# Kernel tuning notes

Hardware: AMD Instinct MI355X
Metric: run time of the kernel (lower is better)

## Reference

```python
import jax, jax.numpy as jnp
import numpy as np

N_NODES = 100000
D_IN = 64
D_OUT = 64
N_EDGES = 1250000


def setup_inputs() -> dict:
    key = jax.random.key(0)
    k_x, k_e, k_wl, k_bl, k_wr = jax.random.split(key, 5)
    x = jax.random.normal(k_x, (N_NODES, D_IN), dtype=jnp.float32)
    edge_index = jax.random.randint(k_e, (2, N_EDGES), 0, N_NODES, dtype=jnp.int64)
    # SAGEConv params: lin_l (neighbor transform, with bias), lin_r (root transform, no bias)
    s_in = 1.0 / np.sqrt(D_IN)
    W_l = jax.random.uniform(k_wl, (D_IN, D_OUT), dtype=jnp.float32, minval=-s_in, maxval=s_in)
    b_l = jax.random.uniform(k_bl, (D_OUT,), dtype=jnp.float32, minval=-s_in, maxval=s_in)
    W_r = jax.random.uniform(k_wr, (D_IN, D_OUT), dtype=jnp.float32, minval=-s_in, maxval=s_in)
    return {"x": x, "edge_index": edge_index, "W_l": W_l, "b_l": b_l, "W_r": W_r}


def reference(x, edge_index, W_l, b_l, W_r):
    # PyG SAGEConv with aggr='add':
    #   out = lin_l(sum_{j in N(i)} x_j) + lin_r(x_i), then tanh
    src = edge_index[0]  # message sources (x_j)
    dst = edge_index[1]  # message targets (i)
    msg = x[src]                                             # [E, D_IN] gather
    aggr = jax.ops.segment_sum(msg, dst, num_segments=x.shape[0])  # [N, D_IN] scatter-add
    out = aggr @ W_l + b_l + x @ W_r                         # [N, D_OUT]
    return jnp.tanh(out)
```

## Files before the change

kernel.cpp:

```cpp
#include <hip/hip_runtime.h>
#include <hip/hip_bf16.h>
#include <hip/hip_fp16.h>

#define N_NODES 100000
#define D 64
#define N_EDGES 1250000

#define RB 64
#define NB 1563
#define FCAP 1536
#define SORT_CAP 1536

#define CB_SHIFT 11
#define NCB 49
#define CCAP 28672
#define FINE_PER_COARSE 32

#define CPAD 16

#define EPB 8192
#define PARTA_BLOCKS ((N_EDGES + EPB - 1) / EPB)
#define SEGS 16

#define TN 64
#define PRE_BLOCKS 1563
#define FUSED_BLOCKS (PARTA_BLOCKS + PRE_BLOCKS)

#define XP 72

typedef unsigned short ushort_t;
typedef _Float16 half_t;
typedef __attribute__((ext_vector_type(8))) _Float16 half8;
typedef __attribute__((ext_vector_type(4))) float floatx4;

__global__ __launch_bounds__(256) void pre_part_kernel(
    const float* __restrict__ x, const float* __restrict__ W_l,
    const float* __restrict__ b_l, const float* __restrict__ W_r,
    ushort_t* __restrict__ y, ushort_t* __restrict__ z,
    const int* __restrict__ src, const int* __restrict__ dst,
    int* __restrict__ ccursor, unsigned* __restrict__ coarse,
    int N, int E)
{
    int t = threadIdx.x;

    if (blockIdx.x < PARTA_BLOCKS) {
        __shared__ int hist[4][NCB];
        __shared__ int wbase[4][NCB];
        const int w = t >> 6;

        if (t < 4 * NCB) ((int*)hist)[t] = 0;
        __syncthreads();

        int base = blockIdx.x * EPB;
        int lim = E - base; if (lim > EPB) lim = EPB;

        for (int i = t; i < lim; i += 256) {
            int d = dst[base + i];
            atomicAdd(&hist[w][d >> CB_SHIFT], 1);
        }
        __syncthreads();

        if (t < NCB) {
            int c0 = hist[0][t], c1 = hist[1][t];
            int c2 = hist[2][t], c3 = hist[3][t];
            int tot = c0 + c1 + c2 + c3;
            int b0 = tot ? atomicAdd(&ccursor[t * CPAD], tot) : 0;
            wbase[0][t] = b0;
            wbase[1][t] = b0 + c0;
            wbase[2][t] = b0 + c0 + c1;
            wbase[3][t] = b0 + c0 + c1 + c2;
        }
        __syncthreads();

        for (int i = t; i < lim; i += 256) {
            int d = dst[base + i];
            int s = src[base + i];
            int b = d >> CB_SHIFT;
            int pos = atomicSub(&hist[w][b], 1) - 1;
            coarse[(size_t)b * CCAP + wbase[w][b] + pos] =
                (unsigned)s | ((unsigned)(d & ((1 << CB_SHIFT) - 1)) << 17);
        }
        return;
    }

    __shared__ half_t sWt[128 * XP];
    __shared__ half_t sXh[TN * XP];

    for (int i = t; i < 64 * 64; i += 256) {
        int k = i >> 6, c = i & 63;
        sWt[c * XP + k]        = (half_t)W_l[i];
        sWt[(64 + c) * XP + k] = (half_t)W_r[i];
    }

    long base = (long)(blockIdx.x - PARTA_BLOCKS) * TN;
    for (int i = t; i < TN * 16; i += 256) {
        int n = i >> 4, q = i & 15;
        long node = base + n;
        float4 v = make_float4(0.f, 0.f, 0.f, 0.f);
        if (node < N) v = ((const float4*)(x + node * D))[q];
        half_t* p = &sXh[n * XP + q * 4];
        p[0] = (half_t)v.x; p[1] = (half_t)v.y;
        p[2] = (half_t)v.z; p[3] = (half_t)v.w;
    }
    __syncthreads();

    const int lane  = t & 63;
    const int w     = t >> 6;
    const int col16 = lane & 15;
    const int quad  = lane >> 4;

    const int nrow = w * 16 + col16;
    half8 a0 = *(half8*)&sXh[nrow * XP + quad * 8];
    half8 a1 = *(half8*)&sXh[nrow * XP + 32 + quad * 8];

    float bias[4];
#pragma unroll
    for (int j = 0; j < 4; j++) bias[j] = b_l[j * 16 + col16];

    long nodeBase = base + w * 16;

#pragma unroll 2
    for (int ct = 0; ct < 8; ct++) {
        int c = ct * 16 + col16;
        half8 b0 = *(half8*)&sWt[c * XP + quad * 8];
        half8 b1 = *(half8*)&sWt[c * XP + 32 + quad * 8];
        floatx4 acc = {0.f, 0.f, 0.f, 0.f};
        acc = __builtin_amdgcn_mfma_f32_16x16x32_f16(a0, b0, acc, 0, 0, 0);
        acc = __builtin_amdgcn_mfma_f32_16x16x32_f16(a1, b1, acc, 0, 0, 0);

        ushort_t* obuf = (ct < 4) ? y : z;
        int cc    = (ct < 4) ? c : (c - 64);
        float badd = (ct < 4) ? 0.f : bias[ct - 4];
#pragma unroll
        for (int r = 0; r < 4; r++) {
            long node = nodeBase + quad * 4 + r;
            if (node < N) {
                half_t hv = (half_t)(acc[r] + badd);
                obuf[node * D + cc] = *(ushort_t*)&hv;
            }
        }
    }
}

__global__ __launch_bounds__(256) void partB_kernel(
    const unsigned* __restrict__ coarse, const int* __restrict__ ccursor,
    int* __restrict__ fcursor, unsigned* __restrict__ fine)
{
    __shared__ int hist[4][FINE_PER_COARSE];
    __shared__ int wbase[4][FINE_PER_COARSE];
    int cb = blockIdx.x >> 4;
    int seg = blockIdx.x & 15;
    int t = threadIdx.x;
    const int w = t >> 6;

    int cnt = ccursor[cb * CPAD];
    int segLen = (cnt + SEGS - 1) / SEGS;
    int beg = seg * segLen;
    int end = beg + segLen; if (end > cnt) end = cnt;

    if (t < 4 * FINE_PER_COARSE) ((int*)hist)[t] = 0;
    __syncthreads();

    const unsigned* __restrict__ slab = coarse + (size_t)cb * CCAP;

    for (int i = beg + t; i < end; i += 256) {
        unsigned e = slab[i];
        atomicAdd(&hist[w][(e >> 17) >> 6], 1);
    }
    __syncthreads();

    if (t < FINE_PER_COARSE) {
        int c0 = hist[0][t], c1 = hist[1][t];
        int c2 = hist[2][t], c3 = hist[3][t];
        int tot = c0 + c1 + c2 + c3;
        int fb = cb * FINE_PER_COARSE + t;
        int b0 = tot ? atomicAdd(&fcursor[fb * CPAD], tot) : 0;
        wbase[0][t] = b0;
        wbase[1][t] = b0 + c0;
        wbase[2][t] = b0 + c0 + c1;
        wbase[3][t] = b0 + c0 + c1 + c2;
    }
    __syncthreads();

    for (int i = beg + t; i < end; i += 256) {
        unsigned e = slab[i];
        unsigned cl = e >> 17;
        int fb_loc = cl >> 6;
        int pos = atomicSub(&hist[w][fb_loc], 1) - 1;
        size_t fb = (size_t)cb * FINE_PER_COARSE + fb_loc;
        fine[fb * FCAP + wbase[w][fb_loc] + pos] =
            (e & 0x1FFFFu) | ((cl & 63u) << 17);
    }
}

__global__ __launch_bounds__(512) void sortgather_kernel(
    const ushort_t* __restrict__ y, const ushort_t* __restrict__ z,
    const unsigned* __restrict__ part, const int* __restrict__ cursor,
    float* __restrict__ out, int N)
{
    __shared__ int sorted[SORT_CAP];
    __shared__ int hist[RB];
    __shared__ int cur[RB];
    __shared__ int begL[RB];

    int b = blockIdx.x;
    int t = threadIdx.x;
    int cnt = cursor[b * CPAD];
    if (cnt > SORT_CAP) cnt = SORT_CAP;
    const unsigned* __restrict__ slab = part + (size_t)b * FCAP;

    unsigned e0 = 0, e1 = 0, e2 = 0;
    int i0 = t, i1 = t + 512, i2 = t + 1024;
    if (i0 < cnt) e0 = slab[i0];
    if (i1 < cnt) e1 = slab[i1];
    if (i2 < cnt) e2 = slab[i2];

    if (t < RB) hist[t] = 0;
    __syncthreads();

    if (i0 < cnt) atomicAdd(&hist[e0 >> 17], 1);
    if (i1 < cnt) atomicAdd(&hist[e1 >> 17], 1);
    if (i2 < cnt) atomicAdd(&hist[e2 >> 17], 1);
    __syncthreads();

    if (t < RB) {
        int v = hist[t];
        int inc = v;
#pragma unroll
        for (int off = 1; off < RB; off <<= 1) {
            int n = __shfl_up(inc, off, RB);
            if (t >= off) inc += n;
        }
        int ex = inc - v;
        cur[t] = ex;
        begL[t] = ex;
    }
    __syncthreads();

    if (i0 < cnt) { int p = atomicAdd(&cur[e0 >> 17], 1); sorted[p] = (int)(e0 & 0x1FFFF); }
    if (i1 < cnt) { int p = atomicAdd(&cur[e1 >> 17], 1); sorted[p] = (int)(e1 & 0x1FFFF); }
    if (i2 < cnt) { int p = atomicAdd(&cur[e2 >> 17], 1); sorted[p] = (int)(e2 & 0x1FFFF); }
    __syncthreads();

    const int g = t >> 3;
    const int f = t & 7;
    int myBeg = begL[g];
    int myDeg = hist[g];

    float2 acc0 = make_float2(0.f, 0.f), acc1 = acc0, acc2 = acc0, acc3 = acc0;

    int i = 0;
    for (; i + 4 <= myDeg; i += 4) {
        int s0 = sorted[myBeg + i];
        int s1 = sorted[myBeg + i + 1];
        int s2 = sorted[myBeg + i + 2];
        int s3 = sorted[myBeg + i + 3];
        uint4 r0 = ((const uint4*)(y + (size_t)s0 * D))[f];
        uint4 r1 = ((const uint4*)(y + (size_t)s1 * D))[f];
        uint4 r2 = ((const uint4*)(y + (size_t)s2 * D))[f];
        uint4 r3 = ((const uint4*)(y + (size_t)s3 * D))[f];
#define ACC(r) { \
        float2 c0 = __half22float2(*(const __half2*)&(r).x); \
        float2 c1 = __half22float2(*(const __half2*)&(r).y); \
        float2 c2 = __half22float2(*(const __half2*)&(r).z); \
        float2 c3 = __half22float2(*(const __half2*)&(r).w); \
        acc0.x += c0.x; acc0.y += c0.y; acc1.x += c1.x; acc1.y += c1.y; \
        acc2.x += c2.x; acc2.y += c2.y; acc3.x += c3.x; acc3.y += c3.y; }
        ACC(r0) ACC(r1) ACC(r2) ACC(r3)
    }
    for (; i < myDeg; i++) {
        int s = sorted[myBeg + i];
        uint4 r = ((const uint4*)(y + (size_t)s * D))[f];
        ACC(r)
    }
#undef ACC

    long gn = (long)b * RB + g;
    if (gn < N) {
        uint4 zr = ((const uint4*)(z + (size_t)gn * D))[f];
        float2 z0 = __half22float2(*(const __half2*)&zr.x);
        float2 z1 = __half22float2(*(const __half2*)&zr.y);
        float2 z2 = __half22float2(*(const __half2*)&zr.z);
        float2 z3 = __half22float2(*(const __half2*)&zr.w);
        float4 o0, o1;
        o0.x = tanhf(acc0.x + z0.x); o0.y = tanhf(acc0.y + z0.y);
        o0.z = tanhf(acc1.x + z1.x); o0.w = tanhf(acc1.y + z1.y);
        o1.x = tanhf(acc2.x + z2.x); o1.y = tanhf(acc2.y + z2.y);
        o1.z = tanhf(acc3.x + z3.x); o1.w = tanhf(acc3.y + z3.y);
        float4* op = (float4*)(out + gn * D);
        op[2 * f] = o0;
        op[2 * f + 1] = o1;
    }
}

extern "C" void kernel_launch(void* const* d_in, const int* in_sizes, int n_in,
                              void* d_out, int out_size, void* d_ws, size_t ws_size,
                              hipStream_t stream) {
    const float* x   = (const float*)d_in[0];
    const int* ei    = (const int*)d_in[1];
    const float* W_l = (const float*)d_in[2];
    const float* b_l = (const float*)d_in[3];
    const float* W_r = (const float*)d_in[4];
    float* out = (float*)d_out;

    const int N = N_NODES;
    const int E = N_EDGES;
    const int* src = ei;
    const int* dst = ei + E;

    char* ws = (char*)d_ws;
    ushort_t* y      = (ushort_t*)(ws);
    ushort_t* z      = (ushort_t*)(ws + 12800000);
    unsigned* coarse = (unsigned*)(ws + 25600000);
    unsigned* fine   = (unsigned*)(ws + 31219712);
    int* ccursor     = (int*)(ws + 40822784);
    int* fcursor     = (int*)(ws + 40825920);

    hipMemsetAsync(ccursor, 0, 103168, stream);

    pre_part_kernel<<<FUSED_BLOCKS, 256, 0, stream>>>(
        x, W_l, b_l, W_r, y, z, src, dst, ccursor, coarse, N, E);
    partB_kernel<<<NCB * SEGS, 256, 0, stream>>>(coarse, ccursor, fcursor, fine);
    sortgather_kernel<<<NB, 512, 0, stream>>>(y, z, fine, fcursor, out, N);
}
```

Measured before the change: 144.2 us.

## Split fused partition/precompute kernel, swap MFMA operands for vectorized fp16 stores

Splits the fused kernel into two launches: a coarse edge-partition kernel (now 4096 edges per block, so more blocks) and a separate node-linear precompute kernel. The precompute swaps the MFMA operands so each lane holds four consecutive output columns of one node. That lets it write packed 8-byte fp16 stores and load the bias as float4, instead of scattered 2-byte stores. The split adds one kernel launch and removes overlap between the two phases. Smaller edge blocks mean more atomics on the global cursor but better load balance.

```diff
diff --git a/kernel.cpp b/kernel.cpp
--- a/kernel.cpp
+++ b/kernel.cpp
@@ -18,13 +18,12 @@
 
 #define CPAD 16
 
-#define EPB 8192
+#define EPB 4096
 #define PARTA_BLOCKS ((N_EDGES + EPB - 1) / EPB)
 #define SEGS 16
 
 #define TN 64
 #define PRE_BLOCKS 1563
-#define FUSED_BLOCKS (PARTA_BLOCKS + PRE_BLOCKS)
 
 #define XP 72
 
@@ -33,58 +32,14 @@
 typedef __attribute__((ext_vector_type(8))) _Float16 half8;
 typedef __attribute__((ext_vector_type(4))) float floatx4;
 
-__global__ __launch_bounds__(256) void pre_part_kernel(
+__global__ __launch_bounds__(256) void pre_kernel(
     const float* __restrict__ x, const float* __restrict__ W_l,
     const float* __restrict__ b_l, const float* __restrict__ W_r,
-    ushort_t* __restrict__ y, ushort_t* __restrict__ z,
-    const int* __restrict__ src, const int* __restrict__ dst,
-    int* __restrict__ ccursor, unsigned* __restrict__ coarse,
-    int N, int E)
+    ushort_t* __restrict__ y, ushort_t* __restrict__ z, int N)
 {
-    int t = threadIdx.x;
-
-    if (blockIdx.x < PARTA_BLOCKS) {
-        __shared__ int hist[4][NCB];
-        __shared__ int wbase[4][NCB];
-        const int w = t >> 6;
-
-        if (t < 4 * NCB) ((int*)hist)[t] = 0;
-        __syncthreads();
-
-        int base = blockIdx.x * EPB;
-        int lim = E - base; if (lim > EPB) lim = EPB;
-
-        for (int i = t; i < lim; i += 256) {
-            int d = dst[base + i];
-            atomicAdd(&hist[w][d >> CB_SHIFT], 1);
-        }
-        __syncthreads();
-
-        if (t < NCB) {
-            int c0 = hist[0][t], c1 = hist[1][t];
-            int c2 = hist[2][t], c3 = hist[3][t];
-            int tot = c0 + c1 + c2 + c3;
-            int b0 = tot ? atomicAdd(&ccursor[t * CPAD], tot) : 0;
-            wbase[0][t] = b0;
-            wbase[1][t] = b0 + c0;
-            wbase[2][t] = b0 + c0 + c1;
-            wbase[3][t] = b0 + c0 + c1 + c2;
-        }
-        __syncthreads();
-
-        for (int i = t; i < lim; i += 256) {
-            int d = dst[base + i];
-            int s = src[base + i];
-            int b = d >> CB_SHIFT;
-            int pos = atomicSub(&hist[w][b], 1) - 1;
-            coarse[(size_t)b * CCAP + wbase[w][b] + pos] =
-                (unsigned)s | ((unsigned)(d & ((1 << CB_SHIFT) - 1)) << 17);
-        }
-        return;
-    }
-
     __shared__ half_t sWt[128 * XP];
     __shared__ half_t sXh[TN * XP];
+    int t = threadIdx.x;
 
     for (int i = t; i < 64 * 64; i += 256) {
         int k = i >> 6, c = i & 63;
@@ -92,7 +47,7 @@
         sWt[(64 + c) * XP + k] = (half_t)W_r[i];
     }
 
-    long base = (long)(blockIdx.x - PARTA_BLOCKS) * TN;
+    long base = (long)blockIdx.x * TN;
     for (int i = t; i < TN * 16; i += 256) {
         int n = i >> 4, q = i & 15;
         long node = base + n;
@@ -102,43 +57,91 @@
         p[0] = (half_t)v.x; p[1] = (half_t)v.y;
         p[2] = (half_t)v.z; p[3] = (half_t)v.w;
     }
-    __syncthreads();
 
     const int lane  = t & 63;
     const int w     = t >> 6;
     const int col16 = lane & 15;
     const int quad  = lane >> 4;
 
+    float4 bq[4];
+#pragma unroll
+    for (int j = 0; j < 4; j++) bq[j] = *(const float4*)(b_l + j * 16 + quad * 4);
+
+    __syncthreads();
+
     const int nrow = w * 16 + col16;
-    half8 a0 = *(half8*)&sXh[nrow * XP + quad * 8];
-    half8 a1 = *(half8*)&sXh[nrow * XP + 32 + quad * 8];
-
-    float bias[4];
-#pragma unroll
-    for (int j = 0; j < 4; j++) bias[j] = b_l[j * 16 + col16];
-
-    long nodeBase = base + w * 16;
+    half8 xb0 = *(half8*)&sXh[nrow * XP + quad * 8];
+    half8 xb1 = *(half8*)&sXh[nrow * XP + 32 + quad * 8];
+
+    long node = base + nrow;
+    bool ok = (node < N);
 
 #pragma unroll 2
     for (int ct = 0; ct < 8; ct++) {
         int c = ct * 16 + col16;
-        half8 b0 = *(half8*)&sWt[c * XP + quad * 8];
-        half8 b1 = *(half8*)&sWt[c * XP + 32 + quad * 8];
+        half8 wa0 = *(half8*)&sWt[c * XP + quad * 8];
+        half8 wa1 = *(half8*)&sWt[c * XP + 32 + quad * 8];
         floatx4 acc = {0.f, 0.f, 0.f, 0.f};
-        acc = __builtin_amdgcn_mfma_f32_16x16x32_f16(a0, b0, acc, 0, 0, 0);
-        acc = __builtin_amdgcn_mfma_f32_16x16x32_f16(a1, b1, acc, 0, 0, 0);
-
-        ushort_t* obuf = (ct < 4) ? y : z;
-        int cc    = (ct < 4) ? c : (c - 64);
-        float badd = (ct < 4) ? 0.f : bias[ct - 4];
-#pragma unroll
-        for (int r = 0; r < 4; r++) {
-            long node = nodeBase + quad * 4 + r;
-            if (node < N) {
-                half_t hv = (half_t)(acc[r] + badd);
-                obuf[node * D + cc] = *(ushort_t*)&hv;
+        acc = __builtin_amdgcn_mfma_f32_16x16x32_f16(wa0, xb0, acc, 0, 0, 0);
+        acc = __builtin_amdgcn_mfma_f32_16x16x32_f16(wa1, xb1, acc, 0, 0, 0);
+
+        if (ok) {
+            int oc = ct * 16 + quad * 4;
+            union { half_t h[4]; uint2 u; } pk;
+            if (ct < 4) {
+                pk.h[0] = (half_t)acc[0]; pk.h[1] = (half_t)acc[1];
+                pk.h[2] = (half_t)acc[2]; pk.h[3] = (half_t)acc[3];
+                *(uint2*)(y + node * D + oc) = pk.u;
+            } else {
+                float4 bv = bq[ct - 4];
+                pk.h[0] = (half_t)(acc[0] + bv.x); pk.h[1] = (half_t)(acc[1] + bv.y);
+                pk.h[2] = (half_t)(acc[2] + bv.z); pk.h[3] = (half_t)(acc[3] + bv.w);
+                *(uint2*)(z + node * D + (oc - 64)) = pk.u;
             }
         }
+    }
+}
+
+__global__ __launch_bounds__(256) void partA_kernel(
+    const int* __restrict__ src, const int* __restrict__ dst,
+    int* __restrict__ ccursor, unsigned* __restrict__ coarse, int E)
+{
+    __shared__ int hist[4][NCB];
+    __shared__ int wbase[4][NCB];
+    int t = threadIdx.x;
+    const int w = t >> 6;
+
+    if (t < 4 * NCB) ((int*)hist)[t] = 0;
+    __syncthreads();
+
+    int base = blockIdx.x * EPB;
+    int lim = E - base; if (lim > EPB) lim = EPB;
+
+    for (int i = t; i < lim; i += 256) {
+        int d = dst[base + i];
+        atomicAdd(&hist[w][d >> CB_SHIFT], 1);
+    }
+    __syncthreads();
+
+    if (t < NCB) {
+        int c0 = hist[0][t], c1 = hist[1][t];
+        int c2 = hist[2][t], c3 = hist[3][t];
+        int tot = c0 + c1 + c2 + c3;
+        int b0 = tot ? atomicAdd(&ccursor[t * CPAD], tot) : 0;
+        wbase[0][t] = b0;
+        wbase[1][t] = b0 + c0;
+        wbase[2][t] = b0 + c0 + c1;
+        wbase[3][t] = b0 + c0 + c1 + c2;
+    }
+    __syncthreads();
+
+    for (int i = t; i < lim; i += 256) {
+        int d = dst[base + i];
+        int s = src[base + i];
+        int b = d >> CB_SHIFT;
+        int pos = atomicSub(&hist[w][b], 1) - 1;
+        coarse[(size_t)b * CCAP + wbase[w][b] + pos] =
+            (unsigned)s | ((unsigned)(d & ((1 << CB_SHIFT) - 1)) << 17);
     }
 }
 
@@ -318,8 +321,8 @@
 
     hipMemsetAsync(ccursor, 0, 103168, stream);
 
-    pre_part_kernel<<<FUSED_BLOCKS, 256, 0, stream>>>(
-        x, W_l, b_l, W_r, y, z, src, dst, ccursor, coarse, N, E);
+    partA_kernel<<<PARTA_BLOCKS, 256, 0, stream>>>(src, dst, ccursor, coarse, E);
+    pre_kernel<<<PRE_BLOCKS, 256, 0, stream>>>(x, W_l, b_l, W_r, y, z, N);
     partB_kernel<<<NCB * SEGS, 256, 0, stream>>>(coarse, ccursor, fcursor, fine);
     sortgather_kernel<<<NB, 512, 0, stream>>>(y, z, fine, fcursor, out, N);
 }
```

Result: slower. 166.3 us (+15.3%).
